# Optimization experiments

Measured on AMD Instinct MI355X. Metric: run time of the kernel, lower is better.

Reference implementation:

```python
import jax, jax.numpy as jnp
import numpy as np
import math

B, N = 1, 768
CS, CZ, CH, H, PQ, PV = 384, 128, 16, 12, 4, 8
EPS = 1e-8


def setup_inputs() -> dict:
    key = jax.random.key(0)
    ks = jax.random.split(key, 12)
    def rn(k, shape, scale=1.0):
        return jax.random.normal(k, shape, dtype=jnp.float32) * scale
    s = rn(ks[0], (B, N, CS))
    z = rn(ks[1], (B, N, N, CZ))
    rot, _ = jnp.linalg.qr(rn(ks[2], (B, N, 3, 3)))  # proper-ish rigid rotations
    rot = rot.astype(jnp.float32)
    trans = rn(ks[3], (B, N, 3))
    sc = 0.02
    Wq = rn(ks[4], (CS, H * CH), sc); bq = jnp.zeros((H * CH,), jnp.float32)
    Wkv = rn(ks[5], (CS, 2 * H * CH), sc); bkv = jnp.zeros((2 * H * CH,), jnp.float32)
    Wqp = rn(ks[6], (CS, H * PQ * 3), sc); bqp = jnp.zeros((H * PQ * 3,), jnp.float32)
    Wkvp = rn(ks[7], (CS, H * (PQ + PV) * 3), sc); bkvp = jnp.zeros((H * (PQ + PV) * 3,), jnp.float32)
    Wb = rn(ks[8], (CZ, H), sc); bb = jnp.zeros((H,), jnp.float32)
    head_w = rn(ks[9], (H,), 0.5)
    Wout = rn(ks[10], (H * (CZ + CH + PV * 4), CS), sc); bout = jnp.zeros((CS,), jnp.float32)
    return dict(s=s, z=z, rot=rot, trans=trans, Wq=Wq, bq=bq, Wkv=Wkv, bkv=bkv,
                Wqp=Wqp, bqp=bqp, Wkvp=Wkvp, bkvp=bkvp, Wb=Wb, bb=bb,
                head_w=head_w, Wout=Wout, bout=bout)


def _split_points(x):
    # [B,N,3*M] -> [B,N,M,3]: first M entries are x-coords, next M y, next M z
    return jnp.stack(jnp.split(x, 3, axis=-1), axis=-1)


def _apply_frame(rot, trans, pts):
    # pts [B,N,M,3] -> R @ p + t
    return jnp.einsum('bnxy,bnmy->bnmx', rot, pts) + trans[:, :, None, :]


def reference(s, z, rot, trans, Wq, bq, Wkv, bkv, Wqp, bqp, Wkvp, bkvp, Wb, bb, head_w, Wout, bout):
    # scalar q/k/v: [B,N,H,CH]
    q = (s @ Wq + bq).reshape(B, N, H, CH)
    kv = (s @ Wkv + bkv).reshape(B, N, H, 2 * CH)
    k, v = kv[..., :CH], kv[..., CH:]

    # point q/k/v in global frame
    q_pts = _apply_frame(rot, trans, _split_points(s @ Wqp + bqp)).reshape(B, N, H, PQ, 3)
    kv_pts = _apply_frame(rot, trans, _split_points(s @ Wkvp + bkvp)).reshape(B, N, H, PQ + PV, 3)
    k_pts, v_pts = kv_pts[..., :PQ, :], kv_pts[..., PQ:, :]

    # pair bias [B,N,N,H]
    b = z @ Wb + bb

    # scalar attention logits [B,H,i,j]
    a = jnp.einsum('bihc,bjhc->bhij', q, k) * math.sqrt(1.0 / (3 * CH))
    a = a + math.sqrt(1.0 / 3) * jnp.transpose(b, (0, 3, 1, 2))

    # point-distance attention: [B,i,j,H,PQ]
    diff = q_pts[:, :, None] - k_pts[:, None]          # [B,i,j,H,PQ,3]
    d2 = jnp.sum(diff * diff, axis=-1)                  # [B,i,j,H,PQ]
    hw = jax.nn.softplus(head_w) * math.sqrt(1.0 / (3 * (PQ * 9.0 / 2)))
    pt_att = -0.5 * jnp.sum(d2 * hw[None, None, None, :, None], axis=-1)  # [B,i,j,H]
    a = a + jnp.transpose(pt_att, (0, 3, 1, 2))

    a = jax.nn.softmax(a, axis=-1)                      # [B,H,i,j]

    # scalar output [B,N,H*CH]
    o = jnp.einsum('bhij,bjhc->bihc', a, v).reshape(B, N, H * CH)

    # point output [B,i,H,PV,3], mapped back into local frame of residue i
    o_pt = jnp.einsum('bhij,bjhpx->bihpx', a, v_pts)
    o_pt = jnp.einsum('bnyx,bnhpy->bnhpx', rot, o_pt - trans[:, :, None, None, :])
    o_pt_norm = jnp.sqrt(jnp.sum(o_pt * o_pt, axis=-1) + EPS).reshape(B, N, H * PV)
    o_pt_flat = o_pt.reshape(B, N, H * PV, 3)

    # pair output [B,N,H*CZ]
    o_pair = jnp.einsum('bhij,bijc->bihc', a, z).reshape(B, N, H * CZ)

    cat = jnp.concatenate(
        [o, o_pt_flat[..., 0], o_pt_flat[..., 1], o_pt_flat[..., 2], o_pt_norm, o_pair], axis=-1)
    return cat @ Wout + bout
```

## Files before the change

kernel.cpp:

```cpp
#include <hip/hip_runtime.h>
#include <hip/hip_bf16.h>
#include <cmath>

#define NN 768
#define CS 384
#define CZ 128
#define CH 16
#define HH 12
#define PQ 4
#define PV 8
#define CATC 2112

typedef __attribute__((ext_vector_type(8))) __bf16 bf16x8;
typedef __attribute__((ext_vector_type(8))) unsigned short us8;
typedef __attribute__((ext_vector_type(4))) float f32x4;

__device__ __forceinline__ unsigned short f2bf(float f) {
  unsigned int u = __builtin_bit_cast(unsigned int, f);
  u += 0x7FFFu + ((u >> 16) & 1u);
  return (unsigned short)(u >> 16);
}
__device__ __forceinline__ float bf2f(unsigned short u) {
  return __builtin_bit_cast(float, ((unsigned int)u) << 16);
}
__device__ __forceinline__ unsigned short nf2bf(float f) {
  __bf16 b = (__bf16)f;
  return __builtin_bit_cast(unsigned short, b);
}

__global__ void k_prep_w(const float* __restrict__ Wq, const float* __restrict__ Wkv,
                         const float* __restrict__ Wqp, const float* __restrict__ Wkvp,
                         const float* __restrict__ Wout,
                         float* __restrict__ Wall, unsigned short* __restrict__ Wout_bf) {
  int g = blockIdx.x*256 + threadIdx.x;
  if (g < 442368) {
    int c = g / 1152, col = g % 1152;
    float v;
    if (col < 192)      v = Wq[(size_t)c*192 + col];
    else if (col < 576) v = Wkv[(size_t)c*384 + (col-192)];
    else if (col < 720) v = Wqp[(size_t)c*144 + (col-576)];
    else                v = Wkvp[(size_t)c*432 + (col-720)];
    Wall[g] = v;
  } else {
    int g2 = g - 442368;
    if (g2 < 811008) Wout_bf[g2] = nf2bf(Wout[g2]);
  }
}

__global__ void __launch_bounds__(384) k_projg(
    const float* __restrict__ s, const float* __restrict__ Wall,
    const float* __restrict__ rot, const float* __restrict__ trans,
    const float* __restrict__ bq, const float* __restrict__ bkv,
    const float* __restrict__ bqp, const float* __restrict__ bkvp,
    float* __restrict__ q, float* __restrict__ kk, float* __restrict__ vv,
    float* __restrict__ qpts, float* __restrict__ kvpts) {
  __shared__ float sl[8][384];
  __shared__ float raw[8][576];
  __shared__ float Rl[8][9];
  __shared__ float Tl[8][3];
  int i0 = blockIdx.x*8, t = threadIdx.x;
  #pragma unroll
  for (int k = 0; k < 8; k++) sl[k][t] = s[(size_t)(i0+k)*CS + t];
  if (t < 72) Rl[t/9][t%9] = rot[(size_t)i0*9 + t];
  else if (t < 96) { int u = t-72; Tl[u/3][u%3] = trans[(size_t)i0*3 + u]; }
  __syncthreads();

  float a0[8], a1[8], a2[8];
  #pragma unroll
  for (int g = 0; g < 8; g++) { a0[g]=0.f; a1[g]=0.f; a2[g]=0.f; }
  {
    const float* w0 = Wall + t;
    const float* w1 = Wall + 384 + t;
    const float* w2 = Wall + 768 + t;
    #pragma unroll 4
    for (int c4 = 0; c4 < 96; c4++) {
      float4 sv[8];
      #pragma unroll
      for (int g = 0; g < 8; g++) sv[g] = *(const float4*)&sl[g][c4*4];
      #pragma unroll
      for (int e = 0; e < 4; e++) {
        int c = c4*4 + e;
        float wv0 = w0[(size_t)c*1152];
        float wv1 = w1[(size_t)c*1152];
        float wv2 = w2[(size_t)c*1152];
        #pragma unroll
        for (int g = 0; g < 8; g++) {
          float svv = (e==0)?sv[g].x:(e==1)?sv[g].y:(e==2)?sv[g].z:sv[g].w;
          a0[g] += svv*wv0; a1[g] += svv*wv1; a2[g] += svv*wv2;
        }
      }
    }
  }
  if (t < 192) {
    float b = bq[t];
    #pragma unroll
    for (int g = 0; g < 8; g++) q[(size_t)(i0+g)*192 + t] = a0[g] + b;
  } else {
    int cc = t - 192;
    float b = bkv[cc];
    int h = cc >> 5, u2 = cc & 31;
    #pragma unroll
    for (int g = 0; g < 8; g++) {
      float v = a0[g] + b;
      if (u2 < 16) kk[(size_t)(i0+g)*192 + h*16 + u2] = v;
      else         vv[(size_t)(i0+g)*192 + h*16 + (u2-16)] = v;
    }
  }
  if (t < 192) {
    int cc = t + 192;
    float b = bkv[cc];
    int h = cc >> 5, u2 = cc & 31;
    #pragma unroll
    for (int g = 0; g < 8; g++) {
      float v = a1[g] + b;
      if (u2 < 16) kk[(size_t)(i0+g)*192 + h*16 + u2] = v;
      else         vv[(size_t)(i0+g)*192 + h*16 + (u2-16)] = v;
    }
  } else if (t < 336) {
    int m = t - 192;
    float b = bqp[m];
    #pragma unroll
    for (int g = 0; g < 8; g++) raw[g][m] = a1[g] + b;
  } else {
    int m2 = t - 336;
    float b = bkvp[m2];
    #pragma unroll
    for (int g = 0; g < 8; g++) raw[g][144 + m2] = a1[g] + b;
  }
  {
    int m2 = t + 48;
    float b = bkvp[m2];
    #pragma unroll
    for (int g = 0; g < 8; g++) raw[g][144 + m2] = a2[g] + b;
  }
  __syncthreads();

  for (int u = t; u < 8*192; u += 384) {
    int g = u / 192, pt = u % 192;
    const float* R = Rl[g];
    const float* T = Tl[g];
    if (pt < 48) {
      float p0 = raw[g][pt], p1 = raw[g][48+pt], p2 = raw[g][96+pt];
      float* d = qpts + ((size_t)(i0+g)*48 + pt)*3;
      d[0] = R[0]*p0 + R[1]*p1 + R[2]*p2 + T[0];
      d[1] = R[3]*p0 + R[4]*p1 + R[5]*p2 + T[1];
      d[2] = R[6]*p0 + R[7]*p1 + R[8]*p2 + T[2];
    } else {
      int m = pt - 48;
      float p0 = raw[g][144+m], p1 = raw[g][288+m], p2 = raw[g][432+m];
      float* d = kvpts + ((size_t)(i0+g)*144 + m)*3;
      d[0] = R[0]*p0 + R[1]*p1 + R[2]*p2 + T[0];
      d[1] = R[3]*p0 + R[4]*p1 + R[5]*p2 + T[1];
      d[2] = R[6]*p0 + R[7]*p1 + R[8]*p2 + T[2];
    }
  }
}

__global__ void k_prep_all(const float* __restrict__ kk, const float* __restrict__ kvpts,
                           const float* __restrict__ Wb, const float* __restrict__ q,
                           const float* __restrict__ qpts, const float* __restrict__ bb,
                           const float* __restrict__ head_w, const float* __restrict__ vv,
                           unsigned short* __restrict__ Bq, unsigned short* __restrict__ afT,
                           unsigned short* __restrict__ augT, unsigned short* __restrict__ Vq) {
  int b = blockIdx.x, t = threadIdx.x;
  if (b < 48) {
    int jt16 = b;
    for (int u = t; u < 768; u += 256) {
      int hp = u >> 6, kg = (u >> 4) & 3, l15 = u & 15;
      int j = jt16*16 + l15;
      unsigned short vals[8];
      #pragma unroll
      for (int e = 0; e < 8; e++) {
        int cc = kg*8 + e;
        float v;
        if (cc < 16) {
          v = kk[(size_t)j*192 + hp*16 + cc];
        } else if (cc < 28) {
          v = kvpts[(size_t)j*432 + hp*36 + (cc-16)];
        } else if (cc == 28) {
          float s2 = 0.f;
          #pragma unroll
          for (int m = 0; m < 12; m++) {
            float d = kvpts[(size_t)j*432 + hp*36 + m];
            s2 += d*d;
          }
          v = s2;
        } else if (cc == 29) {
          v = 1.0f;
        } else {
          v = 0.f;
        }
        vals[e] = f2bf(v);
      }
      *(us8*)(Bq + ((size_t)(jt16*12 + hp)*64 + kg*16 + l15)*8) = *(const us8*)vals;
    }
    if (b == 0) {
      int kg = t >> 6, l15 = (t >> 2) & 15, ks = t & 3;
      unsigned short vals[8];
      #pragma unroll
      for (int kc = 0; kc < 8; kc++) {
        vals[kc] = (l15 < 12)
          ? f2bf(0.5773502691896258f * Wb[(size_t)(ks*32 + kg*8 + kc)*12 + l15])
          : (unsigned short)0;
      }
      *(us8*)(afT + (size_t)t*8) = *(const us8*)vals;
    }
  } else if (b < 240) {
    int g = (b-48)*256 + t;
    int i = g >> 6, kg = (g >> 4) & 3, l15 = g & 15;
    const float sc1 = 0.14433756729740643f;
    const float sc3 = 0.5773502691896258f;
    float hw = (l15 < 12) ? log1pf(expf(head_w[l15])) * 0.13608276348795434f : 0.f;
    unsigned short vals[8];
    #pragma unroll
    for (int e = 0; e < 8; e++) {
      int idx = kg*8 + e;
      float v = 0.f;
      if (l15 < 12) {
        if (idx < 16) v = sc1 * q[(size_t)i*192 + l15*16 + idx];
        else if (idx < 28) v = hw * qpts[(size_t)i*144 + l15*12 + (idx-16)];
        else if (idx == 28) v = -0.5f * hw;
        else if (idx == 29) {
          float s2 = 0.f;
          #pragma unroll
          for (int m = 0; m < 12; m++) {
            float d = qpts[(size_t)i*144 + l15*12 + m];
            s2 += d*d;
          }
          v = sc3 * bb[l15] - 0.5f * hw * s2;
        }
      }
      vals[e] = f2bf(v);
    }
    *(us8*)(augT + (size_t)g*8) = *(const us8*)vals;
  } else {
    int g = (b-240)*256 + t;
    int l15 = g & 15;
    int kg  = (g >> 4) & 3;
    int r2  = g >> 6;
    int ks  = r2 % 24;
    int hn  = r2 / 24;
    int nt  = hn % 3;
    int h   = hn / 3;
    int col = nt*16 + l15;
    unsigned short vals[8];
    #pragma unroll
    for (int e = 0; e < 8; e++) {
      int j = ks*32 + kg*8 + e;
      float v = 0.f;
      if (col < 16)      v = vv[(size_t)j*192 + h*16 + col];
      else if (col < 40) v = kvpts[(size_t)j*432 + h*36 + 12 + (col-16)];
      vals[e] = f2bf(v);
    }
    *(us8*)(Vq + (size_t)g*8) = *(const us8*)vals;
  }
}

#define PL2 136
__global__ void __launch_bounds__(512) k_zpass(
    const float* __restrict__ z, const unsigned short* __restrict__ Bq,
    const unsigned short* __restrict__ afT, const unsigned short* __restrict__ augT,
    unsigned short* __restrict__ p_bf, float* __restrict__ Pp,
    float* __restrict__ msbuf) {
  __shared__ unsigned short zt[128*128];
  __shared__ unsigned short p_l[16*PL2];
  __shared__ float redm[8][16];
  __shared__ float reds[8][16];
  int jt = blockIdx.x, i = blockIdx.y, t = threadIdx.x;
  int w = t >> 6, l = t & 63, kg = l >> 4, l15 = l & 15;
  const us8* afT8 = (const us8*)afT;
  const us8* augT8 = (const us8*)augT;
  const us8* Bq8 = (const us8*)Bq;
  us8 zero8 = {0,0,0,0,0,0,0,0};

  us8 af[4];
  #pragma unroll
  for (int ks = 0; ks < 4; ks++) af[ks] = afT8[(kg*16 + l15)*4 + ks];
  us8 aug = augT8[((size_t)i*4 + kg)*16 + l15];

  int jloc = w*16 + l15;
  int jcol = jt*128 + jloc;
  const float* zr = z + ((size_t)i*NN + jcol)*CZ;
  f32x4 accz = {0.f,0.f,0.f,0.f};
  f32x4 aa0 = {0.f,0.f,0.f,0.f}, aa1 = {0.f,0.f,0.f,0.f}, aa2 = {0.f,0.f,0.f,0.f};
  #pragma unroll
  for (int ks = 0; ks < 4; ks++) {
    float4 z0 = *(const float4*)(zr + ks*32 + kg*8);
    float4 z1 = *(const float4*)(zr + ks*32 + kg*8 + 4);
    bf16x8 bv;
    bv[0] = (__bf16)z0.x; bv[1] = (__bf16)z0.y; bv[2] = (__bf16)z0.z; bv[3] = (__bf16)z0.w;
    bv[4] = (__bf16)z1.x; bv[5] = (__bf16)z1.y; bv[6] = (__bf16)z1.z; bv[7] = (__bf16)z1.w;
    us8 bu = __builtin_bit_cast(us8, bv);
    #pragma unroll
    for (int e = 0; e < 8; e++) {
      int c = ks*32 + kg*8 + e;
      int js = (jloc + 16*((c>>3)&3) + 8*(c&7)) & 127;
      zt[c*128 + js] = bu[e];
    }
    accz = __builtin_amdgcn_mfma_f32_16x16x32_bf16(
        __builtin_bit_cast(bf16x8, af[ks]), bv, accz, 0, 0, 0);
  }
  int jtile = jt*8 + w;
  #pragma unroll
  for (int hp = 0; hp < 12; hp++) {
    us8 bqv = Bq8[(size_t)(jtile*12 + hp)*64 + kg*16 + l15];
    us8 sel = (l15 == hp) ? aug : zero8;
    f32x4* dst = (hp < 4) ? &aa0 : (hp < 8) ? &aa1 : &aa2;
    *dst = __builtin_amdgcn_mfma_f32_16x16x32_bf16(
        __builtin_bit_cast(bf16x8, sel), __builtin_bit_cast(bf16x8, bqv), *dst, 0, 0, 0);
  }
  f32x4 lg = (accz + aa0) + (aa1 + aa2);

  float mr[4];
  #pragma unroll
  for (int r = 0; r < 4; r++) {
    float m = lg[r];
    #pragma unroll
    for (int off = 1; off < 16; off <<= 1) m = fmaxf(m, __shfl_xor(m, off));
    mr[r] = m;
  }
  if (l15 == 0) {
    #pragma unroll
    for (int r = 0; r < 4; r++) redm[w][kg*4+r] = mr[r];
  }
  __syncthreads();
  float er[4], mloc[4], sr[4];
  #pragma unroll
  for (int r = 0; r < 4; r++) {
    int h = kg*4 + r;
    float m = redm[0][h];
    #pragma unroll
    for (int ww = 1; ww < 8; ww++) m = fmaxf(m, redm[ww][h]);
    mloc[r] = m;
    float e = expf(lg[r] - m);
    er[r] = e;
    float s = e;
    #pragma unroll
    for (int off = 1; off < 16; off <<= 1) s += __shfl_xor(s, off);
    sr[r] = s;
  }
  if (l15 == 0) {
    #pragma unroll
    for (int r = 0; r < 4; r++) reds[w][kg*4+r] = sr[r];
  }
  #pragma unroll
  for (int r = 0; r < 4; r++) {
    int row = kg*4 + r;
    p_l[row*PL2 + jloc] = (kg < 3) ? nf2bf(er[r]) : (unsigned short)0;
  }
  __syncthreads();
  if (w == 0 && l15 == 0 && kg < 3) {
    #pragma unroll
    for (int r = 0; r < 4; r++) {
      int h = kg*4 + r;
      float s_loc = reds[0][h] + reds[1][h] + reds[2][h] + reds[3][h]
                  + reds[4][h] + reds[5][h] + reds[6][h] + reds[7][h];
      msbuf[((size_t)i*6 + jt)*24 + h]      = mloc[r];
      msbuf[((size_t)i*6 + jt)*24 + 12 + h] = s_loc;
    }
  }

  {
    const us8* pl8 = (const us8*)p_l;
    us8* pg8 = (us8*)(p_bf + (size_t)i*12*768);
    if (t < 192) {
      int h = t >> 4, c8 = t & 15;
      pg8[h*96 + jt*16 + c8] = pl8[h*17 + c8];
    }
  }

  {
    const us8* pl8 = (const us8*)p_l;
    f32x4 acc = {0.f,0.f,0.f,0.f};
    int c = w*16 + l15;
    int off = 16*((c>>3)&3) + 8*(c&7);
    #pragma unroll
    for (int ks = 0; ks < 4; ks++) {
      us8 av = pl8[l15*17 + ks*4 + kg];
      us8 b = *(const us8*)(zt + c*128 + ((ks*32 + kg*8 + off) & 127));
      acc = __builtin_amdgcn_mfma_f32_16x16x32_bf16(
          __builtin_bit_cast(bf16x8, av), __builtin_bit_cast(bf16x8, b), acc, 0, 0, 0);
    }
    #pragma unroll
    for (int r = 0; r < 4; r++) {
      int h = kg*4 + r;
      if (h < 12)
        Pp[(((size_t)i*6 + jt)*12 + h)*128 + c] = acc[r];
    }
  }
}

__global__ void k_comb(const float* __restrict__ Pp, const float* __restrict__ msbuf,
                       unsigned short* __restrict__ p_bf, float* __restrict__ cat) {
  __shared__ float alpha[12][6];
  int i = blockIdx.x, t = threadIdx.x;
  if (t < 12) {
    int h = t;
    float ml[6];
    float m = -1e30f;
    #pragma unroll
    for (int jt = 0; jt < 6; jt++) {
      ml[jt] = msbuf[((size_t)i*6 + jt)*24 + h];
      m = fmaxf(m, ml[jt]);
    }
    float s = 0.f;
    float al[6];
    #pragma unroll
    for (int jt = 0; jt < 6; jt++) {
      al[jt] = expf(ml[jt] - m);
      s += msbuf[((size_t)i*6 + jt)*24 + 12 + h] * al[jt];
    }
    float invs = 1.0f / s;
    #pragma unroll
    for (int jt = 0; jt < 6; jt++) alpha[h][jt] = al[jt] * invs;
  }
  __syncthreads();
  for (int u = t; u < 1536; u += 256) {
    int h = u >> 7, c = u & 127;
    float acc = 0.f;
    #pragma unroll
    for (int jt = 0; jt < 6; jt++)
      acc += Pp[(((size_t)i*6 + jt)*12 + h)*128 + c] * alpha[h][jt];
    cat[(size_t)i*CATC + 576 + h*128 + c] = acc;
  }
  us8* pg8 = (us8*)(p_bf + (size_t)i*12*768);
  for (int u = t; u < 1152; u += 256) {
    int h = u / 96, c8 = u % 96, jt = c8 >> 4;
    float a = alpha[h][jt];
    us8 v = pg8[h*96 + c8];
    #pragma unroll
    for (int e = 0; e < 8; e++) v[e] = nf2bf(bf2f(v[e]) * a);
    pg8[h*96 + c8] = v;
  }
}

__global__ void k_ov(const unsigned short* __restrict__ p_bf,
                     const unsigned short* __restrict__ Vq,
                     const float* __restrict__ rot, const float* __restrict__ trans,
                     float* __restrict__ cat) {
  __shared__ float opt[16][28];
  __shared__ float Rl[16][9];
  __shared__ float Tl[16][3];
  int it = blockIdx.x, h = blockIdx.y, t = threadIdx.x;
  int i0 = it*16;
  int w = t >> 6, l = t & 63, kg = l >> 4, l15 = l & 15;
  if (t < 144) Rl[t/9][t%9] = rot[(size_t)(i0 + t/9)*9 + (t%9)];
  if (t >= 192 && t < 240) {
    int u = t - 192;
    Tl[u/3][u%3] = trans[(size_t)(i0 + u/3)*3 + (u%3)];
  }
  f32x4 acc = {0.f,0.f,0.f,0.f};
  if (w < 3) {
    const unsigned short* prow = p_bf + ((size_t)(i0 + l15)*12 + h)*768 + kg*8;
    const us8* vq = (const us8*)Vq + (size_t)(h*3 + w)*24*64 + kg*16 + l15;
    for (int ks = 0; ks < 24; ks++) {
      us8 av = *(const us8*)(prow + ks*32);
      us8 bv = vq[(size_t)ks*64];
      acc = __builtin_amdgcn_mfma_f32_16x16x32_bf16(
          __builtin_bit_cast(bf16x8, av), __builtin_bit_cast(bf16x8, bv), acc, 0, 0, 0);
    }
  }
  if (w == 0) {
    #pragma unroll
    for (int r = 0; r < 4; r++)
      cat[(size_t)(i0 + kg*4 + r)*CATC + h*16 + l15] = acc[r];
  } else if (w == 1) {
    #pragma unroll
    for (int r = 0; r < 4; r++) opt[kg*4 + r][l15] = acc[r];
  } else if (w == 2) {
    if (l15 < 8) {
      #pragma unroll
      for (int r = 0; r < 4; r++) opt[kg*4 + r][16 + l15] = acc[r];
    }
  }
  __syncthreads();
  if (t < 128) {
    int ip = t >> 3, p = t & 7;
    float x0 = opt[ip][p*3+0] - Tl[ip][0];
    float x1 = opt[ip][p*3+1] - Tl[ip][1];
    float x2 = opt[ip][p*3+2] - Tl[ip][2];
    const float* R = Rl[ip];
    float ox = R[0]*x0 + R[3]*x1 + R[6]*x2;
    float oy = R[1]*x0 + R[4]*x1 + R[7]*x2;
    float oz = R[2]*x0 + R[5]*x1 + R[8]*x2;
    float nrm = sqrtf(ox*ox + oy*oy + oz*oz + 1e-8f);
    float* c = cat + (size_t)(i0 + ip)*CATC;
    int m = h*8 + p;
    c[192 + m] = ox; c[288 + m] = oy; c[384 + m] = oz; c[480 + m] = nrm;
  }
}

#define OROWS 3
__global__ void k_out(const float* __restrict__ cat, const unsigned short* __restrict__ Wout_bf,
                      const float* __restrict__ bout, float* __restrict__ out) {
  __shared__ float cl[OROWS*CATC];
  int i0 = blockIdx.x*OROWS, t = threadIdx.x;
  for (int idx = t; idx < OROWS*CATC; idx += 384) cl[idx] = cat[(size_t)i0*CATC + idx];
  __syncthreads();
  float acc[OROWS];
  #pragma unroll
  for (int g = 0; g < OROWS; g++) acc[g] = 0.f;
  for (int r = 0; r < CATC; r += 8) {
    float wv[8];
    #pragma unroll
    for (int u = 0; u < 8; u++) wv[u] = bf2f(Wout_bf[(size_t)(r+u)*384 + t]);
    #pragma unroll
    for (int u = 0; u < 8; u++) {
      #pragma unroll
      for (int g = 0; g < OROWS; g++) acc[g] += cl[g*CATC + r + u] * wv[u];
    }
  }
  float bo = bout[t];
  #pragma unroll
  for (int g = 0; g < OROWS; g++) out[(size_t)(i0+g)*384 + t] = acc[g] + bo;
}

extern "C" void kernel_launch(void* const* d_in, const int* in_sizes, int n_in,
                              void* d_out, int out_size, void* d_ws, size_t ws_size,
                              hipStream_t stream) {
  const float* s      = (const float*)d_in[0];
  const float* z      = (const float*)d_in[1];
  const float* rot    = (const float*)d_in[2];
  const float* trans  = (const float*)d_in[3];
  const float* Wq     = (const float*)d_in[4];
  const float* bq     = (const float*)d_in[5];
  const float* Wkv    = (const float*)d_in[6];
  const float* bkv    = (const float*)d_in[7];
  const float* Wqp    = (const float*)d_in[8];
  const float* bqp    = (const float*)d_in[9];
  const float* Wkvp   = (const float*)d_in[10];
  const float* bkvp   = (const float*)d_in[11];
  const float* Wb     = (const float*)d_in[12];
  const float* bb     = (const float*)d_in[13];
  const float* head_w = (const float*)d_in[14];
  const float* Wout   = (const float*)d_in[15];
  const float* bout   = (const float*)d_in[16];
  float* out = (float*)d_out;

  float* ws    = (float*)d_ws;
  float* q     = ws;
  float* kk    = q     + 147456;
  float* vv    = kk    + 147456;
  float* qpts  = vv    + 147456;
  float* kvpts = qpts  + 110592;
  unsigned short* p_bf = (unsigned short*)(kvpts + 331776);
  float* cat   = (float*)(p_bf + 7077888);
  unsigned short* Bq  = (unsigned short*)(cat + 1622016);
  unsigned short* Vq  = Bq + 294912;
  unsigned short* afT = Vq + 884736;
  unsigned short* augT= afT + 2048;
  float* Pp    = (float*)(augT + 393216);
  float* msbuf = Pp + 7077888;
  float* Wall  = msbuf + 110592;
  unsigned short* Wout_bf = (unsigned short*)(Wall + 442368);

  k_prep_w<<<4896, 256, 0, stream>>>(Wq, Wkv, Wqp, Wkvp, Wout, Wall, Wout_bf);
  k_projg<<<96, 384, 0, stream>>>(s, Wall, rot, trans, bq, bkv, bqp, bkvp,
                                  q, kk, vv, qpts, kvpts);
  k_prep_all<<<672, 256, 0, stream>>>(kk, kvpts, Wb, q, qpts, bb, head_w, vv,
                                      Bq, afT, augT, Vq);
  k_zpass<<<dim3(6, 768), 512, 0, stream>>>(z, Bq, afT, augT, p_bf, Pp, msbuf);
  k_comb<<<768, 256, 0, stream>>>(Pp, msbuf, p_bf, cat);
  k_ov<<<dim3(48, 12), 256, 0, stream>>>(p_bf, Vq, rot, trans, cat);
  k_out<<<256, 384, 0, stream>>>(cat, Wout_bf, bout, out);
}
```

Before: 303.4 us.

## Fuse split-softmax combine into k_ov and drop weight-repack kernel

Removes the k_prep_w kernel. k_projg now reads Wq/Wkv/Wqp/Wkvp directly with per-thread strides, and the Wout bf16 conversion moves into extra blocks of k_prep_all. The k_comb kernel is folded into k_ov: each block computes the per-row rescale factors from msbuf, scales the bf16 probabilities on the fly before the MFMA, and writes the pair-output combine itself. This saves two launches and a read-modify-write pass over p_bf. In exchange, k_projg's weight loads are less uniform and k_ov carries more work.

Result: no change. 305.0 us (+0.5%).

```diff
diff --git a/kernel.cpp b/kernel.cpp
--- a/kernel.cpp
+++ b/kernel.cpp
@@ -28,27 +28,10 @@
   return __builtin_bit_cast(unsigned short, b);
 }
 
-__global__ void k_prep_w(const float* __restrict__ Wq, const float* __restrict__ Wkv,
-                         const float* __restrict__ Wqp, const float* __restrict__ Wkvp,
-                         const float* __restrict__ Wout,
-                         float* __restrict__ Wall, unsigned short* __restrict__ Wout_bf) {
-  int g = blockIdx.x*256 + threadIdx.x;
-  if (g < 442368) {
-    int c = g / 1152, col = g % 1152;
-    float v;
-    if (col < 192)      v = Wq[(size_t)c*192 + col];
-    else if (col < 576) v = Wkv[(size_t)c*384 + (col-192)];
-    else if (col < 720) v = Wqp[(size_t)c*144 + (col-576)];
-    else                v = Wkvp[(size_t)c*432 + (col-720)];
-    Wall[g] = v;
-  } else {
-    int g2 = g - 442368;
-    if (g2 < 811008) Wout_bf[g2] = nf2bf(Wout[g2]);
-  }
-}
-
 __global__ void __launch_bounds__(384) k_projg(
-    const float* __restrict__ s, const float* __restrict__ Wall,
+    const float* __restrict__ s,
+    const float* __restrict__ Wq, const float* __restrict__ Wkv,
+    const float* __restrict__ Wqp, const float* __restrict__ Wkvp,
     const float* __restrict__ rot, const float* __restrict__ trans,
     const float* __restrict__ bq, const float* __restrict__ bkv,
     const float* __restrict__ bqp, const float* __restrict__ bkvp,
@@ -65,29 +48,34 @@
   else if (t < 96) { int u = t-72; Tl[u/3][u%3] = trans[(size_t)i0*3 + u]; }
   __syncthreads();
 
+  const float* w0; int s0_, c0_;
+  const float* w1; int s1_, c1_;
+  const float* w2; int s2_, c2_;
+  if (t < 192) { w0 = Wq;   s0_ = 192; c0_ = t; }
+  else         { w0 = Wkv;  s0_ = 384; c0_ = t - 192; }
+  if (t < 192)      { w1 = Wkv;  s1_ = 384; c1_ = t + 192; }
+  else if (t < 336) { w1 = Wqp;  s1_ = 144; c1_ = t - 192; }
+  else              { w1 = Wkvp; s1_ = 432; c1_ = t - 336; }
+  w2 = Wkvp; s2_ = 432; c2_ = t + 48;
+
   float a0[8], a1[8], a2[8];
   #pragma unroll
   for (int g = 0; g < 8; g++) { a0[g]=0.f; a1[g]=0.f; a2[g]=0.f; }
-  {
-    const float* w0 = Wall + t;
-    const float* w1 = Wall + 384 + t;
-    const float* w2 = Wall + 768 + t;
-    #pragma unroll 4
-    for (int c4 = 0; c4 < 96; c4++) {
-      float4 sv[8];
+  #pragma unroll 4
+  for (int c4 = 0; c4 < 96; c4++) {
+    float4 sv[8];
+    #pragma unroll
+    for (int g = 0; g < 8; g++) sv[g] = *(const float4*)&sl[g][c4*4];
+    #pragma unroll
+    for (int e = 0; e < 4; e++) {
+      int c = c4*4 + e;
+      float wv0 = w0[(size_t)c*s0_ + c0_];
+      float wv1 = w1[(size_t)c*s1_ + c1_];
+      float wv2 = w2[(size_t)c*s2_ + c2_];
       #pragma unroll
-      for (int g = 0; g < 8; g++) sv[g] = *(const float4*)&sl[g][c4*4];
-      #pragma unroll
-      for (int e = 0; e < 4; e++) {
-        int c = c4*4 + e;
-        float wv0 = w0[(size_t)c*1152];
-        float wv1 = w1[(size_t)c*1152];
-        float wv2 = w2[(size_t)c*1152];
-        #pragma unroll
-        for (int g = 0; g < 8; g++) {
-          float svv = (e==0)?sv[g].x:(e==1)?sv[g].y:(e==2)?sv[g].z:sv[g].w;
-          a0[g] += svv*wv0; a1[g] += svv*wv1; a2[g] += svv*wv2;
-        }
+      for (int g = 0; g < 8; g++) {
+        float svv = (e==0)?sv[g].x:(e==1)?sv[g].y:(e==2)?sv[g].z:sv[g].w;
+        a0[g] += svv*wv0; a1[g] += svv*wv1; a2[g] += svv*wv2;
       }
     }
   }
@@ -160,8 +148,10 @@
                            const float* __restrict__ Wb, const float* __restrict__ q,
                            const float* __restrict__ qpts, const float* __restrict__ bb,
                            const float* __restrict__ head_w, const float* __restrict__ vv,
+                           const float* __restrict__ Wout,
                            unsigned short* __restrict__ Bq, unsigned short* __restrict__ afT,
-                           unsigned short* __restrict__ augT, unsigned short* __restrict__ Vq) {
+                           unsigned short* __restrict__ augT, unsigned short* __restrict__ Vq,
+                           unsigned short* __restrict__ Wout_bf) {
   int b = blockIdx.x, t = threadIdx.x;
   if (b < 48) {
     int jt16 = b;
@@ -233,7 +223,7 @@
       vals[e] = f2bf(v);
     }
     *(us8*)(augT + (size_t)g*8) = *(const us8*)vals;
-  } else {
+  } else if (b < 672) {
     int g = (b-240)*256 + t;
     int l15 = g & 15;
     int kg  = (g >> 4) & 3;
@@ -253,6 +243,9 @@
       vals[e] = f2bf(v);
     }
     *(us8*)(Vq + (size_t)g*8) = *(const us8*)vals;
+  } else {
+    int g = (b-672)*256 + t;
+    if (g < 811008) Wout_bf[g] = nf2bf(Wout[g]);
   }
 }
 
@@ -390,54 +383,12 @@
   }
 }
 
-__global__ void k_comb(const float* __restrict__ Pp, const float* __restrict__ msbuf,
-                       unsigned short* __restrict__ p_bf, float* __restrict__ cat) {
-  __shared__ float alpha[12][6];
-  int i = blockIdx.x, t = threadIdx.x;
-  if (t < 12) {
-    int h = t;
-    float ml[6];
-    float m = -1e30f;
-    #pragma unroll
-    for (int jt = 0; jt < 6; jt++) {
-      ml[jt] = msbuf[((size_t)i*6 + jt)*24 + h];
-      m = fmaxf(m, ml[jt]);
-    }
-    float s = 0.f;
-    float al[6];
-    #pragma unroll
-    for (int jt = 0; jt < 6; jt++) {
-      al[jt] = expf(ml[jt] - m);
-      s += msbuf[((size_t)i*6 + jt)*24 + 12 + h] * al[jt];
-    }
-    float invs = 1.0f / s;
-    #pragma unroll
-    for (int jt = 0; jt < 6; jt++) alpha[h][jt] = al[jt] * invs;
-  }
-  __syncthreads();
-  for (int u = t; u < 1536; u += 256) {
-    int h = u >> 7, c = u & 127;
-    float acc = 0.f;
-    #pragma unroll
-    for (int jt = 0; jt < 6; jt++)
-      acc += Pp[(((size_t)i*6 + jt)*12 + h)*128 + c] * alpha[h][jt];
-    cat[(size_t)i*CATC + 576 + h*128 + c] = acc;
-  }
-  us8* pg8 = (us8*)(p_bf + (size_t)i*12*768);
-  for (int u = t; u < 1152; u += 256) {
-    int h = u / 96, c8 = u % 96, jt = c8 >> 4;
-    float a = alpha[h][jt];
-    us8 v = pg8[h*96 + c8];
-    #pragma unroll
-    for (int e = 0; e < 8; e++) v[e] = nf2bf(bf2f(v[e]) * a);
-    pg8[h*96 + c8] = v;
-  }
-}
-
 __global__ void k_ov(const unsigned short* __restrict__ p_bf,
                      const unsigned short* __restrict__ Vq,
+                     const float* __restrict__ Pp, const float* __restrict__ msbuf,
                      const float* __restrict__ rot, const float* __restrict__ trans,
                      float* __restrict__ cat) {
+  __shared__ float alpha[16][6];
   __shared__ float opt[16][28];
   __shared__ float Rl[16][9];
   __shared__ float Tl[16][3];
@@ -449,15 +400,42 @@
     int u = t - 192;
     Tl[u/3][u%3] = trans[(size_t)(i0 + u/3)*3 + (u%3)];
   }
+  if (t >= 240 && t < 256) {
+    int iloc = t - 240;
+    float ml[6], sl[6];
+    float m = -1e30f;
+    #pragma unroll
+    for (int jt = 0; jt < 6; jt++) {
+      ml[jt] = msbuf[((size_t)(i0+iloc)*6 + jt)*24 + h];
+      sl[jt] = msbuf[((size_t)(i0+iloc)*6 + jt)*24 + 12 + h];
+      m = fmaxf(m, ml[jt]);
+    }
+    float s = 0.f;
+    float al[6];
+    #pragma unroll
+    for (int jt = 0; jt < 6; jt++) {
+      al[jt] = expf(ml[jt] - m);
+      s += sl[jt] * al[jt];
+    }
+    float invs = 1.0f / s;
+    #pragma unroll
+    for (int jt = 0; jt < 6; jt++) alpha[iloc][jt] = al[jt] * invs;
+  }
+  __syncthreads();
+
   f32x4 acc = {0.f,0.f,0.f,0.f};
   if (w < 3) {
     const unsigned short* prow = p_bf + ((size_t)(i0 + l15)*12 + h)*768 + kg*8;
     const us8* vq = (const us8*)Vq + (size_t)(h*3 + w)*24*64 + kg*16 + l15;
     for (int ks = 0; ks < 24; ks++) {
       us8 av = *(const us8*)(prow + ks*32);
+      float a = alpha[l15][ks >> 2];
+      bf16x8 avs;
+      #pragma unroll
+      for (int e = 0; e < 8; e++) avs[e] = (__bf16)(bf2f(av[e]) * a);
       us8 bv = vq[(size_t)ks*64];
       acc = __builtin_amdgcn_mfma_f32_16x16x32_bf16(
-          __builtin_bit_cast(bf16x8, av), __builtin_bit_cast(bf16x8, bv), acc, 0, 0, 0);
+          avs, __builtin_bit_cast(bf16x8, bv), acc, 0, 0, 0);
     }
   }
   if (w == 0) {
@@ -472,6 +450,14 @@
       #pragma unroll
       for (int r = 0; r < 4; r++) opt[kg*4 + r][16 + l15] = acc[r];
     }
+  }
+  for (int u = t; u < 2048; u += 256) {
+    int iloc = u >> 7, c = u & 127;
+    float a2 = 0.f;
+    #pragma unroll
+    for (int jt = 0; jt < 6; jt++)
+      a2 += Pp[(((size_t)(i0+iloc)*6 + jt)*12 + h)*128 + c] * alpha[iloc][jt];
+    cat[(size_t)(i0+iloc)*CATC + 576 + h*128 + c] = a2;
   }
   __syncthreads();
   if (t < 128) {
@@ -551,16 +537,13 @@
   unsigned short* augT= afT + 2048;
   float* Pp    = (float*)(augT + 393216);
   float* msbuf = Pp + 7077888;
-  float* Wall  = msbuf + 110592;
-  unsigned short* Wout_bf = (unsigned short*)(Wall + 442368);
-
-  k_prep_w<<<4896, 256, 0, stream>>>(Wq, Wkv, Wqp, Wkvp, Wout, Wall, Wout_bf);
-  k_projg<<<96, 384, 0, stream>>>(s, Wall, rot, trans, bq, bkv, bqp, bkvp,
-                                  q, kk, vv, qpts, kvpts);
-  k_prep_all<<<672, 256, 0, stream>>>(kk, kvpts, Wb, q, qpts, bb, head_w, vv,
-                                      Bq, afT, augT, Vq);
+  unsigned short* Wout_bf = (unsigned short*)(msbuf + 110592);
+
+  k_projg<<<96, 384, 0, stream>>>(s, Wq, Wkv, Wqp, Wkvp, rot, trans,
+                                  bq, bkv, bqp, bkvp, q, kk, vv, qpts, kvpts);
+  k_prep_all<<<3840, 256, 0, stream>>>(kk, kvpts, Wb, q, qpts, bb, head_w, vv,
+                                       Wout, Bq, afT, augT, Vq, Wout_bf);
   k_zpass<<<dim3(6, 768), 512, 0, stream>>>(z, Bq, afT, augT, p_bf, Pp, msbuf);
-  k_comb<<<768, 256, 0, stream>>>(Pp, msbuf, p_bf, cat);
-  k_ov<<<dim3(48, 12), 256, 0, stream>>>(p_bf, Vq, rot, trans, cat);
+  k_ov<<<dim3(48, 12), 256, 0, stream>>>(p_bf, Vq, Pp, msbuf, rot, trans, cat);
   k_out<<<256, 384, 0, stream>>>(cat, Wout_bf, bout, out);
 }
```

## Fuse softmax combine into z-pass via last-block atomic counter

Applied to the files above, without the earlier changes.

Removes the separate k_comb kernel. Each k_zpass block increments a per-row atomic counter, and the last of the six column-tile blocks for row i merges the partial max/sum statistics, writes the pair output into cat, and rescales p_bf. This saves one kernel launch and its tail, at the cost of a threadfence plus an atomic per block and a serial tail inside the last block. The counters are zeroed in k_prep_w on each call.

Result: slower. 743.9 us (+145.2%).

```diff
diff --git a/kernel.cpp b/kernel.cpp
--- a/kernel.cpp
+++ b/kernel.cpp
@@ -31,7 +31,8 @@
 __global__ void k_prep_w(const float* __restrict__ Wq, const float* __restrict__ Wkv,
                          const float* __restrict__ Wqp, const float* __restrict__ Wkvp,
                          const float* __restrict__ Wout,
-                         float* __restrict__ Wall, unsigned short* __restrict__ Wout_bf) {
+                         float* __restrict__ Wall, unsigned short* __restrict__ Wout_bf,
+                         int* __restrict__ cnt) {
   int g = blockIdx.x*256 + threadIdx.x;
   if (g < 442368) {
     int c = g / 1152, col = g % 1152;
@@ -45,6 +46,7 @@
     int g2 = g - 442368;
     if (g2 < 811008) Wout_bf[g2] = nf2bf(Wout[g2]);
   }
+  if (g < 768) cnt[g] = 0;
 }
 
 __global__ void __launch_bounds__(384) k_projg(
@@ -261,11 +263,13 @@
     const float* __restrict__ z, const unsigned short* __restrict__ Bq,
     const unsigned short* __restrict__ afT, const unsigned short* __restrict__ augT,
     unsigned short* __restrict__ p_bf, float* __restrict__ Pp,
-    float* __restrict__ msbuf) {
+    float* __restrict__ msbuf, int* __restrict__ cnt, float* __restrict__ cat) {
   __shared__ unsigned short zt[128*128];
   __shared__ unsigned short p_l[16*PL2];
   __shared__ float redm[8][16];
   __shared__ float reds[8][16];
+  __shared__ float alpha[12][6];
+  __shared__ int lastflag;
   int jt = blockIdx.x, i = blockIdx.y, t = threadIdx.x;
   int w = t >> 6, l = t & 63, kg = l >> 4, l15 = l & 15;
   const us8* afT8 = (const us8*)afT;
@@ -388,49 +392,54 @@
         Pp[(((size_t)i*6 + jt)*12 + h)*128 + c] = acc[r];
     }
   }
-}
-
-__global__ void k_comb(const float* __restrict__ Pp, const float* __restrict__ msbuf,
-                       unsigned short* __restrict__ p_bf, float* __restrict__ cat) {
-  __shared__ float alpha[12][6];
-  int i = blockIdx.x, t = threadIdx.x;
-  if (t < 12) {
-    int h = t;
-    float ml[6];
-    float m = -1e30f;
-    #pragma unroll
-    for (int jt = 0; jt < 6; jt++) {
-      ml[jt] = msbuf[((size_t)i*6 + jt)*24 + h];
-      m = fmaxf(m, ml[jt]);
-    }
-    float s = 0.f;
-    float al[6];
-    #pragma unroll
-    for (int jt = 0; jt < 6; jt++) {
-      al[jt] = expf(ml[jt] - m);
-      s += msbuf[((size_t)i*6 + jt)*24 + 12 + h] * al[jt];
-    }
-    float invs = 1.0f / s;
-    #pragma unroll
-    for (int jt = 0; jt < 6; jt++) alpha[h][jt] = al[jt] * invs;
-  }
-  __syncthreads();
-  for (int u = t; u < 1536; u += 256) {
-    int h = u >> 7, c = u & 127;
-    float acc = 0.f;
-    #pragma unroll
-    for (int jt = 0; jt < 6; jt++)
-      acc += Pp[(((size_t)i*6 + jt)*12 + h)*128 + c] * alpha[h][jt];
-    cat[(size_t)i*CATC + 576 + h*128 + c] = acc;
-  }
-  us8* pg8 = (us8*)(p_bf + (size_t)i*12*768);
-  for (int u = t; u < 1152; u += 256) {
-    int h = u / 96, c8 = u % 96, jt = c8 >> 4;
-    float a = alpha[h][jt];
-    us8 v = pg8[h*96 + c8];
-    #pragma unroll
-    for (int e = 0; e < 8; e++) v[e] = nf2bf(bf2f(v[e]) * a);
-    pg8[h*96 + c8] = v;
+
+  __syncthreads();
+  if (t == 0) {
+    __threadfence();
+    int old = atomicAdd(&cnt[i], 1);
+    lastflag = (old == 5) ? 1 : 0;
+    if (lastflag) __threadfence();
+  }
+  __syncthreads();
+  if (lastflag) {
+    if (t < 12) {
+      int h = t;
+      float ml[6];
+      float m = -1e30f;
+      #pragma unroll
+      for (int j2 = 0; j2 < 6; j2++) {
+        ml[j2] = msbuf[((size_t)i*6 + j2)*24 + h];
+        m = fmaxf(m, ml[j2]);
+      }
+      float s = 0.f;
+      float al[6];
+      #pragma unroll
+      for (int j2 = 0; j2 < 6; j2++) {
+        al[j2] = expf(ml[j2] - m);
+        s += msbuf[((size_t)i*6 + j2)*24 + 12 + h] * al[j2];
+      }
+      float invs = 1.0f / s;
+      #pragma unroll
+      for (int j2 = 0; j2 < 6; j2++) alpha[h][j2] = al[j2] * invs;
+    }
+    __syncthreads();
+    for (int u = t; u < 1536; u += 512) {
+      int h = u >> 7, c = u & 127;
+      float acc = 0.f;
+      #pragma unroll
+      for (int j2 = 0; j2 < 6; j2++)
+        acc += Pp[(((size_t)i*6 + j2)*12 + h)*128 + c] * alpha[h][j2];
+      cat[(size_t)i*CATC + 576 + h*128 + c] = acc;
+    }
+    us8* pg8 = (us8*)(p_bf + (size_t)i*12*768);
+    for (int u = t; u < 1152; u += 512) {
+      int h = u / 96, c8 = u % 96, j2 = c8 >> 4;
+      float a = alpha[h][j2];
+      us8 v = pg8[h*96 + c8];
+      #pragma unroll
+      for (int e = 0; e < 8; e++) v[e] = nf2bf(bf2f(v[e]) * a);
+      pg8[h*96 + c8] = v;
+    }
   }
 }
 
@@ -553,14 +562,14 @@
   float* msbuf = Pp + 7077888;
   float* Wall  = msbuf + 110592;
   unsigned short* Wout_bf = (unsigned short*)(Wall + 442368);
-
-  k_prep_w<<<4896, 256, 0, stream>>>(Wq, Wkv, Wqp, Wkvp, Wout, Wall, Wout_bf);
+  int* cnt = (int*)(Wout_bf + 811008);
+
+  k_prep_w<<<4896, 256, 0, stream>>>(Wq, Wkv, Wqp, Wkvp, Wout, Wall, Wout_bf, cnt);
   k_projg<<<96, 384, 0, stream>>>(s, Wall, rot, trans, bq, bkv, bqp, bkvp,
                                   q, kk, vv, qpts, kvpts);
   k_prep_all<<<672, 256, 0, stream>>>(kk, kvpts, Wb, q, qpts, bb, head_w, vv,
                                       Bq, afT, augT, Vq);
-  k_zpass<<<dim3(6, 768), 512, 0, stream>>>(z, Bq, afT, augT, p_bf, Pp, msbuf);
-  k_comb<<<768, 256, 0, stream>>>(Pp, msbuf, p_bf, cat);
+  k_zpass<<<dim3(6, 768), 512, 0, stream>>>(z, Bq, afT, augT, p_bf, Pp, msbuf, cnt, cat);
   k_ov<<<dim3(48, 12), 256, 0, stream>>>(p_bf, Vq, rot, trans, cat);
   k_out<<<256, 384, 0, stream>>>(cat, Wout_bf, bout, out);
 }
```
